# Optimization experiments

Hardware: AMD Instinct MI355X
Metric: run time of the kernel (lower is better)

Reference implementation:

```python
import jax, jax.numpy as jnp
import numpy as np

N_NODES = 100000
N_EDGES = 1600000
D_IN, D_HID, D_OUT = 32, 64, 32


def gcn_conv(x, src, dst, W, b, n_nodes):
    """PyG-style GCNConv: x @ W, add self-loops, symmetric deg^-1/2 norm, scatter-add, + bias."""
    h = x @ W  # [N, d_out]
    ones = jnp.ones(src.shape[0], dtype=h.dtype)
    # in-degree at dst, +1 for the implicit self-loop
    deg = jax.ops.segment_sum(ones, dst, num_segments=n_nodes) + 1.0  # [N]
    dinv_sqrt = jax.lax.rsqrt(deg)
    norm = dinv_sqrt[src] * dinv_sqrt[dst]  # [E]
    agg = jax.ops.segment_sum(h[src] * norm[:, None], dst, num_segments=n_nodes)  # [N, d_out]
    agg = agg + h * (dinv_sqrt * dinv_sqrt)[:, None]  # self-loop term: deg^-1 * h_i
    return agg + b


def setup_inputs() -> dict:
    key = jax.random.key(0)
    ks = jax.random.split(key, 5)
    x = jax.random.normal(ks[0], (N_NODES, D_IN), dtype=jnp.float32)
    edge_index = jax.random.randint(ks[1], (2, N_EDGES), 0, N_NODES, dtype=jnp.int64)
    # Glorot-ish init for GCN weights
    W1 = jax.random.normal(ks[2], (D_IN, D_HID), dtype=jnp.float32) * (1.0 / np.sqrt(D_IN))
    b1 = jnp.zeros((D_HID,), dtype=jnp.float32)
    W2 = jax.random.normal(ks[3], (D_HID, D_OUT), dtype=jnp.float32) * (1.0 / np.sqrt(D_HID))
    b2 = jnp.zeros((D_OUT,), dtype=jnp.float32)
    return {"x": x, "edge_index": edge_index, "W1": W1, "b1": b1, "W2": W2, "b2": b2}


def reference(x, edge_index, W1, b1, W2, b2):
    src, dst = edge_index[0], edge_index[1]
    h = jax.nn.relu(gcn_conv(x, src, dst, W1, b1, N_NODES))
    h = gcn_conv(h, src, dst, W2, b2, N_NODES)
    # per-edge score: gather-multiply-sum
    logits = jnp.sum(h[src] * h[dst], axis=-1)  # [E]
    return logits
```

## Files before the change

### kernel.cpp

```cpp
#include <hip/hip_runtime.h>
#include <hip/hip_fp16.h>

#define N_NODES 100000
#define N_EDGES 1600000
#define D_IN 32
#define D_HID 64
#define D_OUT 32
#define CAP 48
#define PGROUPS 250
#define PGSIZE 400
#define PBINCAP 7200
#define PTILE 8192

__global__ void __launch_bounds__(512) partition_kernel(
    const int* __restrict__ src, const int* __restrict__ dst,
    int* __restrict__ gcur, int2* __restrict__ bins, int E) {
    __shared__ int lcnt[PGROUPS];
    __shared__ int lbase[PGROUPS];
    for (int t = threadIdx.x; t < PGROUPS; t += 512) lcnt[t] = 0;
    __syncthreads();
    int base = blockIdx.x * PTILE + threadIdx.x * 16;
    int s[16], d[16], g[16], p[16];
    int nloc = 0;
    if (base < E) nloc = min(16, E - base);
    if (nloc == 16) {
#pragma unroll
        for (int q = 0; q < 4; ++q) {
            int4 sv = *(const int4*)(src + base + 4 * q);
            int4 dv = *(const int4*)(dst + base + 4 * q);
            s[4*q+0] = sv.x; s[4*q+1] = sv.y; s[4*q+2] = sv.z; s[4*q+3] = sv.w;
            d[4*q+0] = dv.x; d[4*q+1] = dv.y; d[4*q+2] = dv.z; d[4*q+3] = dv.w;
        }
#pragma unroll
        for (int k = 0; k < 16; ++k) {
            g[k] = d[k] / PGSIZE;
            p[k] = atomicAdd(&lcnt[g[k]], 1);
        }
    } else {
        for (int k = 0; k < nloc; ++k) { s[k] = src[base + k]; d[k] = dst[base + k]; }
        for (int k = 0; k < nloc; ++k) {
            g[k] = d[k] / PGSIZE;
            p[k] = atomicAdd(&lcnt[g[k]], 1);
        }
    }
    __syncthreads();
    for (int t = threadIdx.x; t < PGROUPS; t += 512)
        lbase[t] = lcnt[t] ? atomicAdd(&gcur[t], lcnt[t]) : 0;
    __syncthreads();
    if (nloc == 16) {
#pragma unroll
        for (int k = 0; k < 16; ++k) {
            int idx = lbase[g[k]] + p[k];
            if (idx < PBINCAP) bins[(size_t)g[k] * PBINCAP + idx] = make_int2(s[k], d[k]);
        }
    } else {
        for (int k = 0; k < nloc; ++k) {
            int idx = lbase[g[k]] + p[k];
            if (idx < PBINCAP) bins[(size_t)g[k] * PBINCAP + idx] = make_int2(s[k], d[k]);
        }
    }
}

__global__ void __launch_bounds__(256) sort_kernel(
    const int2* __restrict__ bins, const int* __restrict__ gcur,
    int* __restrict__ cnt, int* __restrict__ csr) {
    __shared__ int lcnt[PGSIZE];
    int g = blockIdx.x;
    for (int t = threadIdx.x; t < PGSIZE; t += 256) lcnt[t] = 0;
    __syncthreads();
    int n = gcur[g];
    if (n > PBINCAP) n = PBINCAP;
    const int2* bin = bins + (size_t)g * PBINCAP;
    int lo = g * PGSIZE;
    int i = threadIdx.x;
    for (; i + 768 < n; i += 1024) {
        int2 e0 = bin[i];
        int2 e1 = bin[i + 256];
        int2 e2 = bin[i + 512];
        int2 e3 = bin[i + 768];
        int p0 = atomicAdd(&lcnt[e0.y - lo], 1);
        int p1 = atomicAdd(&lcnt[e1.y - lo], 1);
        int p2 = atomicAdd(&lcnt[e2.y - lo], 1);
        int p3 = atomicAdd(&lcnt[e3.y - lo], 1);
        if (p0 < CAP) csr[(size_t)e0.y * CAP + p0] = e0.x;
        if (p1 < CAP) csr[(size_t)e1.y * CAP + p1] = e1.x;
        if (p2 < CAP) csr[(size_t)e2.y * CAP + p2] = e2.x;
        if (p3 < CAP) csr[(size_t)e3.y * CAP + p3] = e3.x;
    }
    for (; i < n; i += 256) {
        int2 e = bin[i];
        int pos = atomicAdd(&lcnt[e.y - lo], 1);
        if (pos < CAP) csr[(size_t)e.y * CAP + pos] = e.x;
    }
    __syncthreads();
    for (int t = threadIdx.x; t < PGSIZE; t += 256) cnt[lo + t] = lcnt[t];
}

__global__ void scale_kernel(const float* __restrict__ x, const int* __restrict__ cnt,
                             __half* __restrict__ xd, int N) {
    int gid = blockIdx.x * 256 + threadIdx.x;
    int n = gid >> 3;
    int c = (gid & 7) * 4;
    if (n >= N) return;
    float di = rsqrtf((float)cnt[n] + 1.0f);
    float4 v = *(const float4*)(x + (size_t)n * D_IN + c);
    __half2 h0 = __floats2half2_rn(v.x * di, v.y * di);
    __half2 h1 = __floats2half2_rn(v.z * di, v.w * di);
    float2 packed = make_float2(*(float*)&h0, *(float*)&h1);
    *(float2*)(xd + (size_t)n * D_IN + c) = packed;
}

#define ACC2(raw) do { __half2* hp_ = (__half2*)&(raw); \
    float2 g0_ = __half22float2(hp_[0]), g1_ = __half22float2(hp_[1]); \
    acc.x += g0_.x; acc.y += g0_.y; acc.z += g1_.x; acc.w += g1_.y; } while (0)

__global__ void __launch_bounds__(256) agg_mlp_kernel(
    const int* __restrict__ cnt, const int* __restrict__ csr,
    const __half* __restrict__ xd,
    const float* __restrict__ W1, const float* __restrict__ b1,
    const float* __restrict__ W2, __half* __restrict__ g2, int N) {
    __shared__ float W1s[D_IN * D_HID];
    __shared__ float W2s[D_HID * D_OUT];
    __shared__ float b1s[D_HID];
    __shared__ float axs[32][36];
    __shared__ float h1s[32][65];
    for (int t = threadIdx.x; t < D_IN * D_HID; t += 256) W1s[t] = W1[t];
    for (int t = threadIdx.x; t < D_HID * D_OUT; t += 256) W2s[t] = W2[t];
    if (threadIdx.x < D_HID) b1s[threadIdx.x] = b1[threadIdx.x];

    int nl = threadIdx.x >> 3;
    int l8 = threadIdx.x & 7;
    int n = blockIdx.x * 32 + nl;
    int c = l8 * 4;
    int cn = cnt[n];
    int m = cn < CAP ? cn : CAP;
    float di = rsqrtf((float)cn + 1.0f);

    float4 acc;
    {
        float2 raw = *(const float2*)(xd + (size_t)n * D_IN + c);
        __half2* hp = (__half2*)&raw;
        float2 f0 = __half22float2(hp[0]), f1 = __half22float2(hp[1]);
        acc = make_float4(f0.x, f0.y, f1.x, f1.y);
    }
    const int4* row4 = (const int4*)(csr + (size_t)n * CAP);
    int i = 0;
    for (; i + 8 <= m; i += 8) {
        int4 sa = row4[(i >> 2) + 0];
        int4 sb = row4[(i >> 2) + 1];
        float2 r0 = *(const float2*)(xd + (size_t)sa.x * D_IN + c);
        float2 r1 = *(const float2*)(xd + (size_t)sa.y * D_IN + c);
        float2 r2 = *(const float2*)(xd + (size_t)sa.z * D_IN + c);
        float2 r3 = *(const float2*)(xd + (size_t)sa.w * D_IN + c);
        float2 r4 = *(const float2*)(xd + (size_t)sb.x * D_IN + c);
        float2 r5 = *(const float2*)(xd + (size_t)sb.y * D_IN + c);
        float2 r6 = *(const float2*)(xd + (size_t)sb.z * D_IN + c);
        float2 r7 = *(const float2*)(xd + (size_t)sb.w * D_IN + c);
        ACC2(r0); ACC2(r1); ACC2(r2); ACC2(r3);
        ACC2(r4); ACC2(r5); ACC2(r6); ACC2(r7);
    }
    for (; i + 4 <= m; i += 4) {
        int4 s4 = row4[i >> 2];
        float2 r0 = *(const float2*)(xd + (size_t)s4.x * D_IN + c);
        float2 r1 = *(const float2*)(xd + (size_t)s4.y * D_IN + c);
        float2 r2 = *(const float2*)(xd + (size_t)s4.z * D_IN + c);
        float2 r3 = *(const float2*)(xd + (size_t)s4.w * D_IN + c);
        ACC2(r0); ACC2(r1); ACC2(r2); ACC2(r3);
    }
    const int* row = csr + (size_t)n * CAP;
    for (; i < m; ++i) {
        float2 raw = *(const float2*)(xd + (size_t)row[i] * D_IN + c);
        ACC2(raw);
    }
    *(float4*)&axs[nl][c] = make_float4(di * acc.x, di * acc.y, di * acc.z, di * acc.w);
    __syncthreads();

#pragma unroll
    for (int jj = 0; jj < 8; ++jj) {
        int j = l8 * 8 + jj;
        float a = b1s[j];
#pragma unroll
        for (int k = 0; k < D_IN; ++k) a += axs[nl][k] * W1s[k * D_HID + j];
        h1s[nl][j] = fmaxf(a, 0.f);
    }
    __syncthreads();

    float o0 = 0.f, o1 = 0.f, o2 = 0.f, o3 = 0.f;
#pragma unroll
    for (int k = 0; k < D_HID; ++k) {
        float hk = h1s[nl][k];
        o0 += hk * W2s[k * D_OUT + c + 0];
        o1 += hk * W2s[k * D_OUT + c + 1];
        o2 += hk * W2s[k * D_OUT + c + 2];
        o3 += hk * W2s[k * D_OUT + c + 3];
    }
    __half2 p0 = __floats2half2_rn(di * o0, di * o1);
    __half2 p1 = __floats2half2_rn(di * o2, di * o3);
    float2 packed = make_float2(*(float*)&p0, *(float*)&p1);
    *(float2*)(g2 + (size_t)n * D_OUT + c) = packed;
}

__global__ void agg2_kernel(const int* __restrict__ cnt, const int* __restrict__ csr,
                            const __half* __restrict__ G, const float* __restrict__ b,
                            __half* __restrict__ OUT, int N) {
    long long gid = (long long)blockIdx.x * blockDim.x + threadIdx.x;
    int n = (int)(gid >> 3);
    int c = ((int)gid & 7) * 4;
    if (n >= N) return;
    int cn = cnt[n];
    int m = cn < CAP ? cn : CAP;
    float4 acc;
    {
        float2 raw = *(const float2*)(G + (long long)n * D_OUT + c);
        __half2* hp = (__half2*)&raw;
        float2 f0 = __half22float2(hp[0]), f1 = __half22float2(hp[1]);
        acc = make_float4(f0.x, f0.y, f1.x, f1.y);
    }
    const int4* row4 = (const int4*)(csr + (long long)n * CAP);
    int i = 0;
    for (; i + 8 <= m; i += 8) {
        int4 sa = row4[(i >> 2) + 0];
        int4 sb = row4[(i >> 2) + 1];
        float2 r0 = *(const float2*)(G + (long long)sa.x * D_OUT + c);
        float2 r1 = *(const float2*)(G + (long long)sa.y * D_OUT + c);
        float2 r2 = *(const float2*)(G + (long long)sa.z * D_OUT + c);
        float2 r3 = *(const float2*)(G + (long long)sa.w * D_OUT + c);
        float2 r4 = *(const float2*)(G + (long long)sb.x * D_OUT + c);
        float2 r5 = *(const float2*)(G + (long long)sb.y * D_OUT + c);
        float2 r6 = *(const float2*)(G + (long long)sb.z * D_OUT + c);
        float2 r7 = *(const float2*)(G + (long long)sb.w * D_OUT + c);
        ACC2(r0); ACC2(r1); ACC2(r2); ACC2(r3);
        ACC2(r4); ACC2(r5); ACC2(r6); ACC2(r7);
    }
    for (; i + 4 <= m; i += 4) {
        int4 s4 = row4[i >> 2];
        float2 r0 = *(const float2*)(G + (long long)s4.x * D_OUT + c);
        float2 r1 = *(const float2*)(G + (long long)s4.y * D_OUT + c);
        float2 r2 = *(const float2*)(G + (long long)s4.z * D_OUT + c);
        float2 r3 = *(const float2*)(G + (long long)s4.w * D_OUT + c);
        ACC2(r0); ACC2(r1); ACC2(r2); ACC2(r3);
    }
    const int* row = csr + (long long)n * CAP;
    for (; i < m; ++i) {
        float2 raw = *(const float2*)(G + (long long)row[i] * D_OUT + c);
        ACC2(raw);
    }
    float di = rsqrtf((float)cn + 1.0f);
    __half2 h0 = __floats2half2_rn(di * acc.x + b[c + 0], di * acc.y + b[c + 1]);
    __half2 h1 = __floats2half2_rn(di * acc.z + b[c + 2], di * acc.w + b[c + 3]);
    float2 packed = make_float2(*(float*)&h0, *(float*)&h1);
    *(float2*)(OUT + (long long)n * D_OUT + c) = packed;
}

__global__ void logits_kernel(const int* __restrict__ src, const int* __restrict__ dst,
                              const __half* __restrict__ H, float* __restrict__ out, int E) {
    long long gid = (long long)blockIdx.x * blockDim.x + threadIdx.x;
    int e = (int)(gid >> 2);
    int c = ((int)gid & 3) * 8;
    if (e >= E) return;
    int s = src[e], d = dst[e];
    float4 ra = *(const float4*)(H + (long long)s * D_OUT + c);
    float4 rb = *(const float4*)(H + (long long)d * D_OUT + c);
    __half2* pa = (__half2*)&ra;
    __half2* pb = (__half2*)&rb;
    float p = 0.f;
#pragma unroll
    for (int k = 0; k < 4; ++k) {
        float2 fa = __half22float2(pa[k]);
        float2 fb = __half22float2(pb[k]);
        p += fa.x * fb.x + fa.y * fb.y;
    }
    p += __shfl_xor(p, 1);
    p += __shfl_xor(p, 2);
    if ((gid & 3) == 0) out[e] = p;
}

extern "C" void kernel_launch(void* const* d_in, const int* in_sizes, int n_in,
                              void* d_out, int out_size, void* d_ws, size_t ws_size,
                              hipStream_t stream) {
    const float* x  = (const float*)d_in[0];
    const int* edge = (const int*)d_in[1];
    const float* W1 = (const float*)d_in[2];
    const float* b1 = (const float*)d_in[3];
    const float* W2 = (const float*)d_in[4];
    const float* b2 = (const float*)d_in[5];
    float* out = (float*)d_out;

    const int* src = edge;
    const int* dst = edge + N_EDGES;

    char* ws = (char*)d_ws;
    int*    gcur = (int*)ws;
    int*    cnt  = gcur + 256;
    int*    csr  = cnt + N_NODES;
    __half* xd   = (__half*)(csr + (size_t)N_NODES * CAP);
    __half* g2h  = xd + (size_t)N_NODES * D_IN;
    __half* h2h  = g2h + (size_t)N_NODES * D_OUT;
    int2*   bins = (int2*)xd;

    hipMemsetAsync(gcur, 0, 256 * sizeof(int), stream);

    partition_kernel<<<(N_EDGES + PTILE - 1) / PTILE, 512, 0, stream>>>(src, dst, gcur, bins, N_EDGES);

    sort_kernel<<<PGROUPS, 256, 0, stream>>>(bins, gcur, cnt, csr);

    scale_kernel<<<(N_NODES * 8 + 255) / 256, 256, 0, stream>>>(x, cnt, xd, N_NODES);

    agg_mlp_kernel<<<N_NODES / 32, 256, 0, stream>>>(cnt, csr, xd, W1, b1, W2, g2h, N_NODES);

    agg2_kernel<<<(N_NODES * 8 + 255) / 256, 256, 0, stream>>>(cnt, csr, g2h, b2, h2h, N_NODES);

    logits_kernel<<<(N_EDGES * 4) / 256, 256, 0, stream>>>(src, dst, h2h, out, N_EDGES);
}
```

Baseline: 206.4 us.

## Aggregate from destination-partitioned bins with LDS atomics instead of building CSR

Removes the per-node CSR build in the sort kernel. Both aggregation layers now read the destination-grouped edge bins directly and accumulate into a shared-memory float tile through LDS atomics, one block per 200-node group. Degree counting and feature scaling are merged into one kernel. The MLP is split out of the first aggregation, so an fp32 intermediate is written to and read back from memory. The aim is to drop the CSR scatter writes, the CAP truncation, and the per-node row loads. The cost is many shared-memory atomics, only 500 blocks, and the extra intermediate buffer traffic.

After: 704.0 us. 3.41x slower.

```diff
diff --git a/kernel.cpp b/kernel.cpp
--- a/kernel.cpp
+++ b/kernel.cpp
@@ -6,10 +6,9 @@
 #define D_IN 32
 #define D_HID 64
 #define D_OUT 32
-#define CAP 48
-#define PGROUPS 250
-#define PGSIZE 400
-#define PBINCAP 7200
+#define PGROUPS 500
+#define PGSIZE 200
+#define PBINCAP 3840
 #define PTILE 8192
 
 __global__ void __launch_bounds__(512) partition_kernel(
@@ -61,62 +60,83 @@
     }
 }
 
-__global__ void __launch_bounds__(256) sort_kernel(
+__global__ void __launch_bounds__(256) count_scale_kernel(
     const int2* __restrict__ bins, const int* __restrict__ gcur,
-    int* __restrict__ cnt, int* __restrict__ csr) {
+    const float* __restrict__ x, int* __restrict__ cnt, __half* __restrict__ xd) {
     __shared__ int lcnt[PGSIZE];
     int g = blockIdx.x;
     for (int t = threadIdx.x; t < PGSIZE; t += 256) lcnt[t] = 0;
     __syncthreads();
-    int n = gcur[g];
-    if (n > PBINCAP) n = PBINCAP;
+    int n = gcur[g]; if (n > PBINCAP) n = PBINCAP;
     const int2* bin = bins + (size_t)g * PBINCAP;
     int lo = g * PGSIZE;
-    int i = threadIdx.x;
-    for (; i + 768 < n; i += 1024) {
+    for (int i = threadIdx.x; i < n; i += 256)
+        atomicAdd(&lcnt[bin[i].y - lo], 1);
+    __syncthreads();
+    for (int t = threadIdx.x; t < PGSIZE; t += 256) cnt[lo + t] = lcnt[t];
+    for (int u = threadIdx.x; u < PGSIZE * 8; u += 256) {
+        int t = u >> 3, c = (u & 7) * 4;
+        int node = lo + t;
+        float di = rsqrtf((float)lcnt[t] + 1.0f);
+        float4 v = *(const float4*)(x + (size_t)node * D_IN + c);
+        __half2 h0 = __floats2half2_rn(v.x * di, v.y * di);
+        __half2 h1 = __floats2half2_rn(v.z * di, v.w * di);
+        float2 packed = make_float2(*(float*)&h0, *(float*)&h1);
+        *(float2*)(xd + (size_t)node * D_IN + c) = packed;
+    }
+}
+
+__global__ void __launch_bounds__(512, 8) agg1_kernel(
+    const int2* __restrict__ bins, const int* __restrict__ gcur,
+    const int* __restrict__ cnt, const __half* __restrict__ xd,
+    float* __restrict__ axf) {
+    __shared__ float acc[PGSIZE][D_IN + 1];
+    int g = blockIdx.x;
+    for (int t = threadIdx.x; t < PGSIZE * (D_IN + 1); t += 512)
+        ((float*)acc)[t] = 0.f;
+    __syncthreads();
+    int n = gcur[g]; if (n > PBINCAP) n = PBINCAP;
+    const int2* bin = bins + (size_t)g * PBINCAP;
+    int lo = g * PGSIZE;
+    int c = (threadIdx.x & 7) * 4;
+    int i = threadIdx.x >> 3;
+#define GATHER1(ev, rv) float2 rv = *(const float2*)(xd + (size_t)(ev).x * D_IN + c)
+#define SCAT1(ev, rv) do { __half2* hp_ = (__half2*)&(rv); \
+        float2 a_ = __half22float2(hp_[0]), b_ = __half22float2(hp_[1]); \
+        int dl_ = (ev).y - lo; \
+        atomicAdd(&acc[dl_][c + 0], a_.x); atomicAdd(&acc[dl_][c + 1], a_.y); \
+        atomicAdd(&acc[dl_][c + 2], b_.x); atomicAdd(&acc[dl_][c + 3], b_.y); } while (0)
+    for (; i + 192 < n; i += 256) {
         int2 e0 = bin[i];
-        int2 e1 = bin[i + 256];
-        int2 e2 = bin[i + 512];
-        int2 e3 = bin[i + 768];
-        int p0 = atomicAdd(&lcnt[e0.y - lo], 1);
-        int p1 = atomicAdd(&lcnt[e1.y - lo], 1);
-        int p2 = atomicAdd(&lcnt[e2.y - lo], 1);
-        int p3 = atomicAdd(&lcnt[e3.y - lo], 1);
-        if (p0 < CAP) csr[(size_t)e0.y * CAP + p0] = e0.x;
-        if (p1 < CAP) csr[(size_t)e1.y * CAP + p1] = e1.x;
-        if (p2 < CAP) csr[(size_t)e2.y * CAP + p2] = e2.x;
-        if (p3 < CAP) csr[(size_t)e3.y * CAP + p3] = e3.x;
-    }
-    for (; i < n; i += 256) {
+        int2 e1 = bin[i + 64];
+        int2 e2 = bin[i + 128];
+        int2 e3 = bin[i + 192];
+        GATHER1(e0, r0); GATHER1(e1, r1); GATHER1(e2, r2); GATHER1(e3, r3);
+        SCAT1(e0, r0); SCAT1(e1, r1); SCAT1(e2, r2); SCAT1(e3, r3);
+    }
+    for (; i < n; i += 64) {
         int2 e = bin[i];
-        int pos = atomicAdd(&lcnt[e.y - lo], 1);
-        if (pos < CAP) csr[(size_t)e.y * CAP + pos] = e.x;
-    }
-    __syncthreads();
-    for (int t = threadIdx.x; t < PGSIZE; t += 256) cnt[lo + t] = lcnt[t];
-}
-
-__global__ void scale_kernel(const float* __restrict__ x, const int* __restrict__ cnt,
-                             __half* __restrict__ xd, int N) {
-    int gid = blockIdx.x * 256 + threadIdx.x;
-    int n = gid >> 3;
-    int c = (gid & 7) * 4;
-    if (n >= N) return;
-    float di = rsqrtf((float)cnt[n] + 1.0f);
-    float4 v = *(const float4*)(x + (size_t)n * D_IN + c);
-    __half2 h0 = __floats2half2_rn(v.x * di, v.y * di);
-    __half2 h1 = __floats2half2_rn(v.z * di, v.w * di);
-    float2 packed = make_float2(*(float*)&h0, *(float*)&h1);
-    *(float2*)(xd + (size_t)n * D_IN + c) = packed;
-}
-
-#define ACC2(raw) do { __half2* hp_ = (__half2*)&(raw); \
-    float2 g0_ = __half22float2(hp_[0]), g1_ = __half22float2(hp_[1]); \
-    acc.x += g0_.x; acc.y += g0_.y; acc.z += g1_.x; acc.w += g1_.y; } while (0)
-
-__global__ void __launch_bounds__(256) agg_mlp_kernel(
-    const int* __restrict__ cnt, const int* __restrict__ csr,
-    const __half* __restrict__ xd,
+        GATHER1(e, r);
+        SCAT1(e, r);
+    }
+    __syncthreads();
+    for (int u = threadIdx.x; u < PGSIZE * 8; u += 512) {
+        int t = u >> 3, cc = (u & 7) * 4;
+        int node = lo + t;
+        float di = rsqrtf((float)cnt[node] + 1.0f);
+        float2 raw = *(const float2*)(xd + (size_t)node * D_IN + cc);
+        __half2* hp = (__half2*)&raw;
+        float2 f0 = __half22float2(hp[0]), f1 = __half22float2(hp[1]);
+        float4 o = make_float4(di * (acc[t][cc + 0] + f0.x), di * (acc[t][cc + 1] + f0.y),
+                               di * (acc[t][cc + 2] + f1.x), di * (acc[t][cc + 3] + f1.y));
+        *(float4*)(axf + (size_t)node * D_IN + cc) = o;
+    }
+#undef GATHER1
+#undef SCAT1
+}
+
+__global__ void __launch_bounds__(256) mlp_kernel(
+    const int* __restrict__ cnt, const float* __restrict__ axf,
     const float* __restrict__ W1, const float* __restrict__ b1,
     const float* __restrict__ W2, __half* __restrict__ g2, int N) {
     __shared__ float W1s[D_IN * D_HID];
@@ -132,47 +152,9 @@
     int l8 = threadIdx.x & 7;
     int n = blockIdx.x * 32 + nl;
     int c = l8 * 4;
-    int cn = cnt[n];
-    int m = cn < CAP ? cn : CAP;
-    float di = rsqrtf((float)cn + 1.0f);
-
-    float4 acc;
-    {
-        float2 raw = *(const float2*)(xd + (size_t)n * D_IN + c);
-        __half2* hp = (__half2*)&raw;
-        float2 f0 = __half22float2(hp[0]), f1 = __half22float2(hp[1]);
-        acc = make_float4(f0.x, f0.y, f1.x, f1.y);
-    }
-    const int4* row4 = (const int4*)(csr + (size_t)n * CAP);
-    int i = 0;
-    for (; i + 8 <= m; i += 8) {
-        int4 sa = row4[(i >> 2) + 0];
-        int4 sb = row4[(i >> 2) + 1];
-        float2 r0 = *(const float2*)(xd + (size_t)sa.x * D_IN + c);
-        float2 r1 = *(const float2*)(xd + (size_t)sa.y * D_IN + c);
-        float2 r2 = *(const float2*)(xd + (size_t)sa.z * D_IN + c);
-        float2 r3 = *(const float2*)(xd + (size_t)sa.w * D_IN + c);
-        float2 r4 = *(const float2*)(xd + (size_t)sb.x * D_IN + c);
-        float2 r5 = *(const float2*)(xd + (size_t)sb.y * D_IN + c);
-        float2 r6 = *(const float2*)(xd + (size_t)sb.z * D_IN + c);
-        float2 r7 = *(const float2*)(xd + (size_t)sb.w * D_IN + c);
-        ACC2(r0); ACC2(r1); ACC2(r2); ACC2(r3);
-        ACC2(r4); ACC2(r5); ACC2(r6); ACC2(r7);
-    }
-    for (; i + 4 <= m; i += 4) {
-        int4 s4 = row4[i >> 2];
-        float2 r0 = *(const float2*)(xd + (size_t)s4.x * D_IN + c);
-        float2 r1 = *(const float2*)(xd + (size_t)s4.y * D_IN + c);
-        float2 r2 = *(const float2*)(xd + (size_t)s4.z * D_IN + c);
-        float2 r3 = *(const float2*)(xd + (size_t)s4.w * D_IN + c);
-        ACC2(r0); ACC2(r1); ACC2(r2); ACC2(r3);
-    }
-    const int* row = csr + (size_t)n * CAP;
-    for (; i < m; ++i) {
-        float2 raw = *(const float2*)(xd + (size_t)row[i] * D_IN + c);
-        ACC2(raw);
-    }
-    *(float4*)&axs[nl][c] = make_float4(di * acc.x, di * acc.y, di * acc.z, di * acc.w);
+    float di = rsqrtf((float)cnt[n] + 1.0f);
+    float4 av = *(const float4*)(axf + (size_t)n * D_IN + c);
+    *(float4*)&axs[nl][c] = av;
     __syncthreads();
 
 #pragma unroll
@@ -200,56 +182,57 @@
     *(float2*)(g2 + (size_t)n * D_OUT + c) = packed;
 }
 
-__global__ void agg2_kernel(const int* __restrict__ cnt, const int* __restrict__ csr,
-                            const __half* __restrict__ G, const float* __restrict__ b,
-                            __half* __restrict__ OUT, int N) {
-    long long gid = (long long)blockIdx.x * blockDim.x + threadIdx.x;
-    int n = (int)(gid >> 3);
-    int c = ((int)gid & 7) * 4;
-    if (n >= N) return;
-    int cn = cnt[n];
-    int m = cn < CAP ? cn : CAP;
-    float4 acc;
-    {
-        float2 raw = *(const float2*)(G + (long long)n * D_OUT + c);
+__global__ void __launch_bounds__(512, 8) agg2_kernel(
+    const int2* __restrict__ bins, const int* __restrict__ gcur,
+    const int* __restrict__ cnt, const __half* __restrict__ G,
+    const float* __restrict__ b, __half* __restrict__ OUT) {
+    __shared__ float acc[PGSIZE][D_OUT + 1];
+    int g = blockIdx.x;
+    for (int t = threadIdx.x; t < PGSIZE * (D_OUT + 1); t += 512)
+        ((float*)acc)[t] = 0.f;
+    __syncthreads();
+    int n = gcur[g]; if (n > PBINCAP) n = PBINCAP;
+    const int2* bin = bins + (size_t)g * PBINCAP;
+    int lo = g * PGSIZE;
+    int c = (threadIdx.x & 7) * 4;
+    int i = threadIdx.x >> 3;
+#define GATHER2(ev, rv) float2 rv = *(const float2*)(G + (size_t)(ev).x * D_OUT + c)
+#define SCAT2(ev, rv) do { __half2* hp_ = (__half2*)&(rv); \
+        float2 a_ = __half22float2(hp_[0]), b_ = __half22float2(hp_[1]); \
+        int dl_ = (ev).y - lo; \
+        atomicAdd(&acc[dl_][c + 0], a_.x); atomicAdd(&acc[dl_][c + 1], a_.y); \
+        atomicAdd(&acc[dl_][c + 2], b_.x); atomicAdd(&acc[dl_][c + 3], b_.y); } while (0)
+    for (; i + 192 < n; i += 256) {
+        int2 e0 = bin[i];
+        int2 e1 = bin[i + 64];
+        int2 e2 = bin[i + 128];
+        int2 e3 = bin[i + 192];
+        GATHER2(e0, r0); GATHER2(e1, r1); GATHER2(e2, r2); GATHER2(e3, r3);
+        SCAT2(e0, r0); SCAT2(e1, r1); SCAT2(e2, r2); SCAT2(e3, r3);
+    }
+    for (; i < n; i += 64) {
+        int2 e = bin[i];
+        GATHER2(e, r);
+        SCAT2(e, r);
+    }
+    __syncthreads();
+    for (int u = threadIdx.x; u < PGSIZE * 8; u += 512) {
+        int t = u >> 3, cc = (u & 7) * 4;
+        int node = lo + t;
+        float di = rsqrtf((float)cnt[node] + 1.0f);
+        float2 raw = *(const float2*)(G + (size_t)node * D_OUT + cc);
         __half2* hp = (__half2*)&raw;
         float2 f0 = __half22float2(hp[0]), f1 = __half22float2(hp[1]);
-        acc = make_float4(f0.x, f0.y, f1.x, f1.y);
-    }
-    const int4* row4 = (const int4*)(csr + (long long)n * CAP);
-    int i = 0;
-    for (; i + 8 <= m; i += 8) {
-        int4 sa = row4[(i >> 2) + 0];
-        int4 sb = row4[(i >> 2) + 1];
-        float2 r0 = *(const float2*)(G + (long long)sa.x * D_OUT + c);
-        float2 r1 = *(const float2*)(G + (long long)sa.y * D_OUT + c);
-        float2 r2 = *(const float2*)(G + (long long)sa.z * D_OUT + c);
-        float2 r3 = *(const float2*)(G + (long long)sa.w * D_OUT + c);
-        float2 r4 = *(const float2*)(G + (long long)sb.x * D_OUT + c);
-        float2 r5 = *(const float2*)(G + (long long)sb.y * D_OUT + c);
-        float2 r6 = *(const float2*)(G + (long long)sb.z * D_OUT + c);
-        float2 r7 = *(const float2*)(G + (long long)sb.w * D_OUT + c);
-        ACC2(r0); ACC2(r1); ACC2(r2); ACC2(r3);
-        ACC2(r4); ACC2(r5); ACC2(r6); ACC2(r7);
-    }
-    for (; i + 4 <= m; i += 4) {
-        int4 s4 = row4[i >> 2];
-        float2 r0 = *(const float2*)(G + (long long)s4.x * D_OUT + c);
-        float2 r1 = *(const float2*)(G + (long long)s4.y * D_OUT + c);
-        float2 r2 = *(const float2*)(G + (long long)s4.z * D_OUT + c);
-        float2 r3 = *(const float2*)(G + (long long)s4.w * D_OUT + c);
-        ACC2(r0); ACC2(r1); ACC2(r2); ACC2(r3);
-    }
-    const int* row = csr + (long long)n * CAP;
-    for (; i < m; ++i) {
-        float2 raw = *(const float2*)(G + (long long)row[i] * D_OUT + c);
-        ACC2(raw);
-    }
-    float di = rsqrtf((float)cn + 1.0f);
-    __half2 h0 = __floats2half2_rn(di * acc.x + b[c + 0], di * acc.y + b[c + 1]);
-    __half2 h1 = __floats2half2_rn(di * acc.z + b[c + 2], di * acc.w + b[c + 3]);
-    float2 packed = make_float2(*(float*)&h0, *(float*)&h1);
-    *(float2*)(OUT + (long long)n * D_OUT + c) = packed;
+        float4 bb = *(const float4*)(b + cc);
+        __half2 h0 = __floats2half2_rn(di * (acc[t][cc + 0] + f0.x) + bb.x,
+                                       di * (acc[t][cc + 1] + f0.y) + bb.y);
+        __half2 h1 = __floats2half2_rn(di * (acc[t][cc + 2] + f1.x) + bb.z,
+                                       di * (acc[t][cc + 3] + f1.y) + bb.w);
+        float2 packed = make_float2(*(float*)&h0, *(float*)&h1);
+        *(float2*)(OUT + (size_t)node * D_OUT + cc) = packed;
+    }
+#undef GATHER2
+#undef SCAT2
 }
 
 __global__ void logits_kernel(const int* __restrict__ src, const int* __restrict__ dst,
@@ -291,24 +274,24 @@
 
     char* ws = (char*)d_ws;
     int*    gcur = (int*)ws;
-    int*    cnt  = gcur + 256;
-    int*    csr  = cnt + N_NODES;
-    __half* xd   = (__half*)(csr + (size_t)N_NODES * CAP);
-    __half* g2h  = xd + (size_t)N_NODES * D_IN;
-    __half* h2h  = g2h + (size_t)N_NODES * D_OUT;
-    int2*   bins = (int2*)xd;
-
-    hipMemsetAsync(gcur, 0, 256 * sizeof(int), stream);
+    int*    cnt  = gcur + 512;
+    int2*   bins = (int2*)(cnt + N_NODES);
+    __half* xd   = (__half*)(bins + (size_t)PGROUPS * PBINCAP);
+    float*  axf  = (float*)(xd + (size_t)N_NODES * D_IN);
+    __half* g2h  = xd;
+    __half* h2h  = (__half*)axf;
+
+    hipMemsetAsync(gcur, 0, 512 * sizeof(int), stream);
 
     partition_kernel<<<(N_EDGES + PTILE - 1) / PTILE, 512, 0, stream>>>(src, dst, gcur, bins, N_EDGES);
 
-    sort_kernel<<<PGROUPS, 256, 0, stream>>>(bins, gcur, cnt, csr);
-
-    scale_kernel<<<(N_NODES * 8 + 255) / 256, 256, 0, stream>>>(x, cnt, xd, N_NODES);
-
-    agg_mlp_kernel<<<N_NODES / 32, 256, 0, stream>>>(cnt, csr, xd, W1, b1, W2, g2h, N_NODES);
-
-    agg2_kernel<<<(N_NODES * 8 + 255) / 256, 256, 0, stream>>>(cnt, csr, g2h, b2, h2h, N_NODES);
+    count_scale_kernel<<<PGROUPS, 256, 0, stream>>>(bins, gcur, x, cnt, xd);
+
+    agg1_kernel<<<PGROUPS, 512, 0, stream>>>(bins, gcur, cnt, xd, axf);
+
+    mlp_kernel<<<N_NODES / 32, 256, 0, stream>>>(cnt, axf, W1, b1, W2, g2h, N_NODES);
+
+    agg2_kernel<<<PGROUPS, 512, 0, stream>>>(bins, gcur, cnt, g2h, b2, h2h);
 
     logits_kernel<<<(N_EDGES * 4) / 256, 256, 0, stream>>>(src, dst, h2h, out, N_EDGES);
 }
```

## Fuse feature scaling into sort, split layer-1 aggregation from MLP, dual accumulators

Applied to the files above, without the earlier changes.

Scaling and fp16 conversion of x now run inside the sort kernel, which already holds per-node degrees in shared memory, so the separate scale launch and its reread of cnt go away. The fused gather+MLP kernel is split into a pure gather kernel that writes fp32 aggregates to workspace and an MLP kernel that reads them. The aim is to keep the gather from being held back by the weight-loading and shared-memory-heavy MLP phase, at the cost of an extra fp32 round trip and one more launch. Both gather loops now alternate between two accumulators to break the add dependency chain, and the workspace buffers are reassigned so the bins region is reused.

Result: slower. 217.8 us (+5.5%).

```diff
diff --git a/kernel.cpp b/kernel.cpp
--- a/kernel.cpp
+++ b/kernel.cpp
@@ -61,9 +61,10 @@
     }
 }
 
-__global__ void __launch_bounds__(256) sort_kernel(
+__global__ void __launch_bounds__(256) sort_scale_kernel(
     const int2* __restrict__ bins, const int* __restrict__ gcur,
-    int* __restrict__ cnt, int* __restrict__ csr) {
+    const float* __restrict__ x,
+    int* __restrict__ cnt, int* __restrict__ csr, __half* __restrict__ xd) {
     __shared__ int lcnt[PGSIZE];
     int g = blockIdx.x;
     for (int t = threadIdx.x; t < PGSIZE; t += 256) lcnt[t] = 0;
@@ -94,49 +95,33 @@
     }
     __syncthreads();
     for (int t = threadIdx.x; t < PGSIZE; t += 256) cnt[lo + t] = lcnt[t];
-}
-
-__global__ void scale_kernel(const float* __restrict__ x, const int* __restrict__ cnt,
-                             __half* __restrict__ xd, int N) {
+    for (int u = threadIdx.x; u < PGSIZE * 8; u += 256) {
+        int t = u >> 3, c = (u & 7) * 4;
+        int node = lo + t;
+        float di = rsqrtf((float)lcnt[t] + 1.0f);
+        float4 v = *(const float4*)(x + (size_t)node * D_IN + c);
+        __half2 h0 = __floats2half2_rn(v.x * di, v.y * di);
+        __half2 h1 = __floats2half2_rn(v.z * di, v.w * di);
+        float2 packed = make_float2(*(float*)&h0, *(float*)&h1);
+        *(float2*)(xd + (size_t)node * D_IN + c) = packed;
+    }
+}
+
+#define ACC2(acc, raw) do { __half2* hp_ = (__half2*)&(raw); \
+    float2 g0_ = __half22float2(hp_[0]), g1_ = __half22float2(hp_[1]); \
+    (acc).x += g0_.x; (acc).y += g0_.y; (acc).z += g1_.x; (acc).w += g1_.y; } while (0)
+
+__global__ void __launch_bounds__(256) agg1_kernel(
+    const int* __restrict__ cnt, const int* __restrict__ csr,
+    const __half* __restrict__ xd, float* __restrict__ axf, int N) {
     int gid = blockIdx.x * 256 + threadIdx.x;
     int n = gid >> 3;
     int c = (gid & 7) * 4;
-    if (n >= N) return;
-    float di = rsqrtf((float)cnt[n] + 1.0f);
-    float4 v = *(const float4*)(x + (size_t)n * D_IN + c);
-    __half2 h0 = __floats2half2_rn(v.x * di, v.y * di);
-    __half2 h1 = __floats2half2_rn(v.z * di, v.w * di);
-    float2 packed = make_float2(*(float*)&h0, *(float*)&h1);
-    *(float2*)(xd + (size_t)n * D_IN + c) = packed;
-}
-
-#define ACC2(raw) do { __half2* hp_ = (__half2*)&(raw); \
-    float2 g0_ = __half22float2(hp_[0]), g1_ = __half22float2(hp_[1]); \
-    acc.x += g0_.x; acc.y += g0_.y; acc.z += g1_.x; acc.w += g1_.y; } while (0)
-
-__global__ void __launch_bounds__(256) agg_mlp_kernel(
-    const int* __restrict__ cnt, const int* __restrict__ csr,
-    const __half* __restrict__ xd,
-    const float* __restrict__ W1, const float* __restrict__ b1,
-    const float* __restrict__ W2, __half* __restrict__ g2, int N) {
-    __shared__ float W1s[D_IN * D_HID];
-    __shared__ float W2s[D_HID * D_OUT];
-    __shared__ float b1s[D_HID];
-    __shared__ float axs[32][36];
-    __shared__ float h1s[32][65];
-    for (int t = threadIdx.x; t < D_IN * D_HID; t += 256) W1s[t] = W1[t];
-    for (int t = threadIdx.x; t < D_HID * D_OUT; t += 256) W2s[t] = W2[t];
-    if (threadIdx.x < D_HID) b1s[threadIdx.x] = b1[threadIdx.x];
-
-    int nl = threadIdx.x >> 3;
-    int l8 = threadIdx.x & 7;
-    int n = blockIdx.x * 32 + nl;
-    int c = l8 * 4;
     int cn = cnt[n];
     int m = cn < CAP ? cn : CAP;
     float di = rsqrtf((float)cn + 1.0f);
 
-    float4 acc;
+    float4 acc, accB = make_float4(0.f, 0.f, 0.f, 0.f);
     {
         float2 raw = *(const float2*)(xd + (size_t)n * D_IN + c);
         __half2* hp = (__half2*)&raw;
@@ -156,8 +141,8 @@
         float2 r5 = *(const float2*)(xd + (size_t)sb.y * D_IN + c);
         float2 r6 = *(const float2*)(xd + (size_t)sb.z * D_IN + c);
         float2 r7 = *(const float2*)(xd + (size_t)sb.w * D_IN + c);
-        ACC2(r0); ACC2(r1); ACC2(r2); ACC2(r3);
-        ACC2(r4); ACC2(r5); ACC2(r6); ACC2(r7);
+        ACC2(acc, r0); ACC2(accB, r1); ACC2(acc, r2); ACC2(accB, r3);
+        ACC2(acc, r4); ACC2(accB, r5); ACC2(acc, r6); ACC2(accB, r7);
     }
     for (; i + 4 <= m; i += 4) {
         int4 s4 = row4[i >> 2];
@@ -165,14 +150,38 @@
         float2 r1 = *(const float2*)(xd + (size_t)s4.y * D_IN + c);
         float2 r2 = *(const float2*)(xd + (size_t)s4.z * D_IN + c);
         float2 r3 = *(const float2*)(xd + (size_t)s4.w * D_IN + c);
-        ACC2(r0); ACC2(r1); ACC2(r2); ACC2(r3);
+        ACC2(acc, r0); ACC2(accB, r1); ACC2(acc, r2); ACC2(accB, r3);
     }
     const int* row = csr + (size_t)n * CAP;
     for (; i < m; ++i) {
         float2 raw = *(const float2*)(xd + (size_t)row[i] * D_IN + c);
-        ACC2(raw);
-    }
-    *(float4*)&axs[nl][c] = make_float4(di * acc.x, di * acc.y, di * acc.z, di * acc.w);
+        ACC2(acc, raw);
+    }
+    float4 o = make_float4(di * (acc.x + accB.x), di * (acc.y + accB.y),
+                           di * (acc.z + accB.z), di * (acc.w + accB.w));
+    *(float4*)(axf + (size_t)n * D_IN + c) = o;
+}
+
+__global__ void __launch_bounds__(256) mlp_kernel(
+    const int* __restrict__ cnt, const float* __restrict__ axf,
+    const float* __restrict__ W1, const float* __restrict__ b1,
+    const float* __restrict__ W2, __half* __restrict__ g2, int N) {
+    __shared__ float W1s[D_IN * D_HID];
+    __shared__ float W2s[D_HID * D_OUT];
+    __shared__ float b1s[D_HID];
+    __shared__ float axs[32][36];
+    __shared__ float h1s[32][65];
+    for (int t = threadIdx.x; t < D_IN * D_HID; t += 256) W1s[t] = W1[t];
+    for (int t = threadIdx.x; t < D_HID * D_OUT; t += 256) W2s[t] = W2[t];
+    if (threadIdx.x < D_HID) b1s[threadIdx.x] = b1[threadIdx.x];
+
+    int nl = threadIdx.x >> 3;
+    int l8 = threadIdx.x & 7;
+    int n = blockIdx.x * 32 + nl;
+    int c = l8 * 4;
+    float di = rsqrtf((float)cnt[n] + 1.0f);
+    float4 av = *(const float4*)(axf + (size_t)n * D_IN + c);
+    *(float4*)&axs[nl][c] = av;
     __syncthreads();
 
 #pragma unroll
@@ -200,16 +209,17 @@
     *(float2*)(g2 + (size_t)n * D_OUT + c) = packed;
 }
 
-__global__ void agg2_kernel(const int* __restrict__ cnt, const int* __restrict__ csr,
-                            const __half* __restrict__ G, const float* __restrict__ b,
-                            __half* __restrict__ OUT, int N) {
+__global__ void __launch_bounds__(256) agg2_kernel(
+    const int* __restrict__ cnt, const int* __restrict__ csr,
+    const __half* __restrict__ G, const float* __restrict__ b,
+    __half* __restrict__ OUT, int N) {
     long long gid = (long long)blockIdx.x * blockDim.x + threadIdx.x;
     int n = (int)(gid >> 3);
     int c = ((int)gid & 7) * 4;
     if (n >= N) return;
     int cn = cnt[n];
     int m = cn < CAP ? cn : CAP;
-    float4 acc;
+    float4 acc, accB = make_float4(0.f, 0.f, 0.f, 0.f);
     {
         float2 raw = *(const float2*)(G + (long long)n * D_OUT + c);
         __half2* hp = (__half2*)&raw;
@@ -229,8 +239,8 @@
         float2 r5 = *(const float2*)(G + (long long)sb.y * D_OUT + c);
         float2 r6 = *(const float2*)(G + (long long)sb.z * D_OUT + c);
         float2 r7 = *(const float2*)(G + (long long)sb.w * D_OUT + c);
-        ACC2(r0); ACC2(r1); ACC2(r2); ACC2(r3);
-        ACC2(r4); ACC2(r5); ACC2(r6); ACC2(r7);
+        ACC2(acc, r0); ACC2(accB, r1); ACC2(acc, r2); ACC2(accB, r3);
+        ACC2(acc, r4); ACC2(accB, r5); ACC2(acc, r6); ACC2(accB, r7);
     }
     for (; i + 4 <= m; i += 4) {
         int4 s4 = row4[i >> 2];
@@ -238,16 +248,18 @@
         float2 r1 = *(const float2*)(G + (long long)s4.y * D_OUT + c);
         float2 r2 = *(const float2*)(G + (long long)s4.z * D_OUT + c);
         float2 r3 = *(const float2*)(G + (long long)s4.w * D_OUT + c);
-        ACC2(r0); ACC2(r1); ACC2(r2); ACC2(r3);
+        ACC2(acc, r0); ACC2(accB, r1); ACC2(acc, r2); ACC2(accB, r3);
     }
     const int* row = csr + (long long)n * CAP;
     for (; i < m; ++i) {
         float2 raw = *(const float2*)(G + (long long)row[i] * D_OUT + c);
-        ACC2(raw);
+        ACC2(acc, raw);
     }
     float di = rsqrtf((float)cn + 1.0f);
-    __half2 h0 = __floats2half2_rn(di * acc.x + b[c + 0], di * acc.y + b[c + 1]);
-    __half2 h1 = __floats2half2_rn(di * acc.z + b[c + 2], di * acc.w + b[c + 3]);
+    __half2 h0 = __floats2half2_rn(di * (acc.x + accB.x) + b[c + 0],
+                                   di * (acc.y + accB.y) + b[c + 1]);
+    __half2 h1 = __floats2half2_rn(di * (acc.z + accB.z) + b[c + 2],
+                                   di * (acc.w + accB.w) + b[c + 3]);
     float2 packed = make_float2(*(float*)&h0, *(float*)&h1);
     *(float2*)(OUT + (long long)n * D_OUT + c) = packed;
 }
@@ -293,20 +305,21 @@
     int*    gcur = (int*)ws;
     int*    cnt  = gcur + 256;
     int*    csr  = cnt + N_NODES;
-    __half* xd   = (__half*)(csr + (size_t)N_NODES * CAP);
-    __half* g2h  = xd + (size_t)N_NODES * D_IN;
-    __half* h2h  = g2h + (size_t)N_NODES * D_OUT;
-    int2*   bins = (int2*)xd;
+    int2*   bins = (int2*)(csr + (size_t)N_NODES * CAP);
+    __half* xd   = (__half*)(bins + (size_t)PGROUPS * PBINCAP);
+    float*  axf  = (float*)bins;
+    __half* g2h  = xd;
+    __half* h2h  = (__half*)bins;
 
     hipMemsetAsync(gcur, 0, 256 * sizeof(int), stream);
 
     partition_kernel<<<(N_EDGES + PTILE - 1) / PTILE, 512, 0, stream>>>(src, dst, gcur, bins, N_EDGES);
 
-    sort_kernel<<<PGROUPS, 256, 0, stream>>>(bins, gcur, cnt, csr);
-
-    scale_kernel<<<(N_NODES * 8 + 255) / 256, 256, 0, stream>>>(x, cnt, xd, N_NODES);
-
-    agg_mlp_kernel<<<N_NODES / 32, 256, 0, stream>>>(cnt, csr, xd, W1, b1, W2, g2h, N_NODES);
+    sort_scale_kernel<<<PGROUPS, 256, 0, stream>>>(bins, gcur, x, cnt, csr, xd);
+
+    agg1_kernel<<<(N_NODES * 8) / 256, 256, 0, stream>>>(cnt, csr, xd, axf, N_NODES);
+
+    mlp_kernel<<<N_NODES / 32, 256, 0, stream>>>(cnt, axf, W1, b1, W2, g2h, N_NODES);
 
     agg2_kernel<<<(N_NODES * 8 + 255) / 256, 256, 0, stream>>>(cnt, csr, g2h, b2, h2h, N_NODES);
 
```
